# Optimization experiments

Hardware: AMD Instinct MI355X
Metric: run time of the kernel (lower is better)

The kernel has to match this reference:

```python
import jax, jax.numpy as jnp
import numpy as np

B, N, E = 512, 714, 4096
VOCAB = 400 + 38333   # cat_len + poi_len
ED = (128 - 3) // 2   # 62
F_IN = 2 * ED + 3     # 127


def setup_inputs() -> dict:
    key = jax.random.key(0)
    ks = jax.random.split(key, 16)
    s = 0.05
    return {
        "ids": jax.random.randint(ks[0], (B, N, 2), 0, VOCAB),
        "cont": jax.random.normal(ks[1], (B, N, 3), jnp.float32),
        "edges": jax.random.randint(ks[2], (B, 2, E), 0, N),
        "emb_table": jax.random.normal(ks[3], (VOCAB, ED), jnp.float32) * 0.02,
        "W1": jax.random.normal(ks[4], (F_IN, 32), jnp.float32) * s,
        "b1": jnp.zeros((32,), jnp.float32),
        "W2": jax.random.normal(ks[5], (32, 32), jnp.float32) * s,
        "b2": jnp.zeros((32,), jnp.float32),
        "W3": jax.random.normal(ks[6], (32, 32), jnp.float32) * s,
        "b3": jnp.zeros((32,), jnp.float32),
        "W4": jax.random.normal(ks[7], (32, 1), jnp.float32) * s,
        "b4": jnp.zeros((1,), jnp.float32),
        "Wf1": jax.random.normal(ks[8], (N, 128), jnp.float32) * s,
        "bf1": jnp.zeros((128,), jnp.float32),
        "Wf2": jax.random.normal(ks[9], (128, 128), jnp.float32) * s,
        "bf2": jnp.zeros((128,), jnp.float32),
    }


def _prep_edges(e):
    # PyG GCNConv: add self-loops, symmetric normalization
    loop = jnp.arange(N)
    row = jnp.concatenate([e[0], loop])           # source j
    col = jnp.concatenate([e[1], loop])           # target i
    deg = jnp.zeros((N,), jnp.float32).at[col].add(1.0)
    dinv = jax.lax.rsqrt(deg)                     # deg >= 1 (self-loops)
    return row, col, dinv[row] * dinv[col]


def _gcn(x, row, col, norm, W, b):
    # x: [N, F_in] -> [N, F_out]; gather-normalize-scatter aggregation
    xw = x @ W
    out = jnp.zeros_like(xw).at[col].add(xw[row] * norm[:, None])
    return out + b


_gcn_b = jax.vmap(_gcn, in_axes=(0, 0, 0, 0, None, None))


def _forward(ids, cont, edges, emb_table, W1, b1, W2, b2, W3, b3, W4, b4,
             Wf1, bf1, Wf2, bf2):
    lrelu = jax.nn.leaky_relu  # torch default slope 0.01
    emb = emb_table[ids.astype(jnp.int32)].reshape(B, N, 2 * ED)  # [B,N,124]
    x = jnp.concatenate([emb, cont], axis=-1)                      # [B,N,127]
    row, col, norm = jax.vmap(_prep_edges)(edges)
    h = lrelu(_gcn_b(x, row, col, norm, W1, b1))
    t = _gcn_b(h, row, col, norm, W2, b2)
    h = lrelu(t) + t
    t = _gcn_b(h, row, col, norm, W3, b3)
    h = lrelu(t) + t
    h = lrelu(_gcn_b(h, row, col, norm, W4, b4))                   # [B,N,1]
    h = h.reshape(B, N)
    h = jax.nn.relu(h @ Wf1 + bf1)
    return jax.nn.relu(h @ Wf2 + bf2)                              # [B,128]


def reference(ids, cont, edges, emb_table, W1, b1, W2, b2, W3, b3, W4, b4,
              Wf1, bf1, Wf2, bf2):
    return _forward(ids, cont, edges, emb_table, W1, b1, W2, b2, W3, b3,
                    W4, b4, Wf1, bf1, Wf2, bf2)
```

## Files before the change

### kernel.cpp

```cpp
#include <hip/hip_runtime.h>
#include <hip/hip_bf16.h>

#define BB 512
#define NN 714
#define EE 4096
#define ED2 62
#define CH 32
#define NT16 45
#define NPAD 720
#define VOCAB 38733
#define NPRE 303
#define ELLR 432
#define ELLB (ELLR*16)

typedef unsigned int u32;
typedef unsigned short u16;
typedef short short8 __attribute__((ext_vector_type(8)));
typedef float float4v __attribute__((ext_vector_type(4)));
typedef _Float16 f16x2 __attribute__((ext_vector_type(2)));
typedef __fp16 fp16x2 __attribute__((ext_vector_type(2)));

__device__ __forceinline__ u32 f2bf(float f) {
  u32 u = __float_as_uint(f);
  return (u + 0x7fffu + ((u >> 16) & 1u)) >> 16;
}
__device__ __forceinline__ u32 pack2(float a, float b) {
  return f2bf(a) | (f2bf(b) << 16);
}
__device__ __forceinline__ f16x2 u2h(u32 x) { union { u32 u; f16x2 h; } c; c.u = x; return c.h; }
__device__ __forceinline__ u32 packh(float a, float b) {
  union { fp16x2 h; u32 u; } c;
  c.h = __builtin_amdgcn_cvt_pkrtz(a, b);
  return c.u;
}

__device__ __forceinline__ int yslot(int node, int q) {
  return (node << 2) | (q ^ ((node >> 1) & 3));
}

__global__ __launch_bounds__(256) void k_setup(const float* __restrict__ emb,
    const float* __restrict__ W1, u32* __restrict__ Tg,
    const int* __restrict__ edges,
    float* __restrict__ dinv, u16* __restrict__ perm_g,
    u16* __restrict__ ell_g, u16* __restrict__ elloff_g)
{
  const int tid = threadIdx.x;
  if (blockIdx.x < NPRE) {
    const int base = blockIdx.x * 128;
    const int lane = tid & 63, wv = tid >> 6;
    const int col = lane & 15, kg = lane >> 4;
    __shared__ __align__(16) unsigned short sX[128 * 64];
    for (int s = tid; s < 1024; s += 256) {
      const int row = s >> 3, ck = s & 7;
      uint4 w = {0, 0, 0, 0};
      if (base + row < VOCAB) {
        const float2* __restrict__ p = (const float2*)(emb + (size_t)(base + row) * ED2 + ck * 8);
        float2 v0 = p[0], v1 = p[1], v2 = p[2];
        float2 v3; v3.x = 0.f; v3.y = 0.f;
        if (ck != 7) v3 = p[3];
        w.x = pack2(v0.x, v0.y); w.y = pack2(v1.x, v1.y);
        w.z = pack2(v2.x, v2.y); w.w = pack2(v3.x, v3.y);
      }
      ((uint4*)sX)[(row * 8 + ck) ^ (row & 7)] = w;
    }
    union { u32 u[4]; short8 v; } A[2][4];
#pragma unroll
    for (int kc = 0; kc < 2; ++kc)
#pragma unroll
      for (int hh = 0; hh < 4; ++hh) {
        const int tbl = hh >> 1;
        const int ch = ((hh & 1) * 16) + col;
#pragma unroll
        for (int jj = 0; jj < 4; ++jj) {
          const int k0 = kc * 32 + kg * 8 + 2 * jj;
          const int k1 = k0 + 1;
          const float wa = (k0 < 62) ? W1[(tbl * 62 + k0) * CH + ch] : 0.f;
          const float wb = (k1 < 62) ? W1[(tbl * 62 + k1) * CH + ch] : 0.f;
          A[kc][hh].u[jj] = pack2(wa, wb);
        }
      }
    __syncthreads();
    for (int t = wv; t < 8; t += 4) {
      const int ln = t * 16 + col;
      float4v acc[4];
#pragma unroll
      for (int hh = 0; hh < 4; ++hh) { acc[hh][0] = 0.f; acc[hh][1] = 0.f; acc[hh][2] = 0.f; acc[hh][3] = 0.f; }
#pragma unroll
      for (int kc = 0; kc < 2; ++kc) {
        const int idx8 = (ln * 8 + kc * 4 + kg) ^ (ln & 7);
        short8 bf = *(const short8*)(sX + idx8 * 8);
#pragma unroll
        for (int hh = 0; hh < 4; ++hh)
          acc[hh] = __builtin_amdgcn_mfma_f32_16x16x32_bf16(A[kc][hh].v, bf, acc[hh], 0, 0, 0);
      }
      const int row = base + ln;
      if (row < VOCAB) {
        u32* op = Tg + (size_t)row * 32;
#pragma unroll
        for (int hh = 0; hh < 4; ++hh) {
          uint2 s0 = { packh(acc[hh][0], acc[hh][1]), packh(acc[hh][2], acc[hh][3]) };
          *(uint2*)(op + hh * 8 + 2 * kg) = s0;
        }
      }
    }
    return;
  }
  const int b = blockIdx.x - NPRE;
  const int* __restrict__ er = edges + (size_t)b * 2 * EE;
  const int* __restrict__ ec = er + EE;
  __shared__ int s_cnt[NN];
  __shared__ int s_a[1024];
  __shared__ int s_b[1024];
  __shared__ u16 s_rows16[EE];
  __shared__ u16 s_perm[NPAD];
  __shared__ u16 s_degP[NPAD];
  __shared__ int s_hist[64];
  __shared__ int s_md[NT16 + 1];

  for (int i = tid; i < NN; i += 256) s_cnt[i] = 0;
  __syncthreads();
  for (int e = tid; e < EE; e += 256) atomicAdd(&s_cnt[ec[e]], 1);
  __syncthreads();
  for (int i = tid; i < 1024; i += 256) s_a[i] = (i < NN) ? s_cnt[i] : 0;
  for (int i = tid; i < NN; i += 256)
    dinv[(size_t)b * NN + i] = rsqrtf((float)(s_cnt[i] + 1));
  __syncthreads();
  int* src = s_a; int* dst = s_b;
  for (int d = 1; d < 1024; d <<= 1) {
    for (int i = tid; i < 1024; i += 256) {
      int v = src[i];
      if (i >= d) v += src[i - d];
      dst[i] = v;
    }
    __syncthreads();
    int* t = src; src = dst; dst = t;
  }
  for (int i = tid; i < NN; i += 256) s_cnt[i] = 0;
  __syncthreads();
  for (int e = tid; e < EE; e += 256) {
    int c = ec[e];
    int p = atomicAdd(&s_cnt[c], 1);
    int base = (c == 0) ? 0 : src[c - 1];
    s_rows16[base + p] = (u16)er[e];
  }
  for (int i = tid; i < 64; i += 256) s_hist[i] = 0;
  for (int i = tid; i < NPAD; i += 256) { s_perm[i] = 0xFFFFu; s_degP[i] = 0; }
  __syncthreads();
  for (int i = tid; i < NN; i += 256) {
    int deg = src[i] - (i ? src[i - 1] : 0);
    atomicAdd(&s_hist[deg < 63 ? deg : 63], 1);
  }
  __syncthreads();
  if (tid < 64) {
    int v = s_hist[tid];
    int incl = v;
#pragma unroll
    for (int d = 1; d < 64; d <<= 1) {
      int o = __shfl_up(incl, d, 64);
      if (tid >= d) incl += o;
    }
    s_hist[tid] = incl - v;
  }
  __syncthreads();
  for (int i = tid; i < NN; i += 256) {
    int deg = src[i] - (i ? src[i - 1] : 0);
    int pos = atomicAdd(&s_hist[deg < 63 ? deg : 63], 1);
    s_perm[pos] = (u16)i;
    s_degP[pos] = (u16)deg;
  }
  __syncthreads();
  for (int i = tid; i < NPAD; i += 256) perm_g[(size_t)b * NPAD + i] = s_perm[i];
  if (tid < NT16) {
    int md = 0;
#pragma unroll
    for (int c = 0; c < 16; ++c) { int d = s_degP[tid * 16 + c]; md = d > md ? d : md; }
    s_md[tid] = (md + 3) & ~3;
  }
  __syncthreads();
  if (tid < 64) {
    int m = (tid < NT16) ? s_md[tid] : 0;
    int incl = m;
#pragma unroll
    for (int d = 1; d < 64; d <<= 1) {
      int o = __shfl_up(incl, d, 64);
      if (tid >= d) incl += o;
    }
    int excl = incl - m;
    if (excl > ELLR) excl = ELLR;
    if (tid < NT16) s_md[tid] = excl;
    if (tid == NT16 - 1) s_md[NT16] = (incl > ELLR) ? ELLR : incl;
  }
  __syncthreads();
  if (tid <= NT16) elloff_g[(size_t)b * (NT16 + 1) + tid] = (u16)s_md[tid];
  {
    const int wv4 = tid >> 6, lane = tid & 63;
    u16* eg = ell_g + (size_t)b * ELLB;
    for (int t = wv4; t < NT16; t += 4) {
      const int base = s_md[t], md4 = s_md[t + 1] - base;
      for (int s = lane; s < md4 * 16; s += 64) {
        const int kk = s >> 4, col = s & 15;
        const int pv = s_perm[t * 16 + col];
        int r = NN;
        if (pv != 0xFFFF) {
          const int deg = s_degP[t * 16 + col];
          if (kk < deg) {
            const int off = pv ? src[pv - 1] : 0;
            r = (int)s_rows16[off + kk];
          }
        }
        eg[base * 16 + s] = (u16)((r << 2) | ((r >> 1) & 3));
      }
    }
  }
}

#define EDGEA(EP, K) { const int a16 = ((int)(EP)[(K) * 16]) ^ kg; \
  uint4 n = sy4[a16]; \
  a0h += u2h(n.x); a1h += u2h(n.y); a2h += u2h(n.z); a3h += u2h(n.w); }
#define EDGEB(EP, K) { const int a16 = ((int)(EP)[(K) * 16]) ^ kg; \
  uint4 n = sy4[a16]; \
  b0h += u2h(n.x); b1h += u2h(n.y); b2h += u2h(n.z); b3h += u2h(n.w); }
#define FLUSH { a0h += b0h; a1h += b1h; a2h += b2h; a3h += b3h; \
  zx[0] += (float)a0h.x; zx[1] += (float)a0h.y; \
  zx[2] += (float)a1h.x; zx[3] += (float)a1h.y; \
  zx[4] += (float)a2h.x; zx[5] += (float)a2h.y; \
  zx[6] += (float)a3h.x; zx[7] += (float)a3h.y; \
  a0h = hz; a1h = hz; a2h = hz; a3h = hz; \
  b0h = hz; b1h = hz; b2h = hz; b3h = hz; }
#define AGG_LOOP(EP) { int kk = 0; \
  while (kk + 16 <= md4) { \
    _Pragma("unroll") for (int e = 0; e < 16; e += 2) { EDGEA(EP, kk + e) EDGEB(EP, kk + e + 1) } \
    FLUSH \
    kk += 16; } \
  if (kk + 8 <= md4) { \
    _Pragma("unroll") for (int e = 0; e < 8; e += 2) { EDGEA(EP, kk + e) EDGEB(EP, kk + e + 1) } \
    FLUSH \
    kk += 8; } \
  if (kk < md4) { \
    _Pragma("unroll") for (int e = 0; e < 4; e += 2) { EDGEA(EP, kk + e) EDGEB(EP, kk + e + 1) } \
    FLUSH } }

template<int ACT>
__device__ __forceinline__ void gcn_pass32(
    u32* __restrict__ sy, const u16* __restrict__ s_ell,
    const u16* __restrict__ s_elloff, const float* __restrict__ s_dv,
    const u16* __restrict__ pvs,
    const int wv, const int col, const int kg,
    const short8 a0v, const short8 a1v, const float* __restrict__ bias8)
{
  const uint4* sy4 = (const uint4*)sy;
  const f16x2 hz = {(_Float16)0, (_Float16)0};
  u32 outs[3][4];
  int nodes[3];
#pragma unroll
  for (int p = 0; p < 3; ++p) {
    const int t = p * 16 + wv;
    const int pv = (t < NT16) ? (int)pvs[p] : 0xFFFF;
    const int node = (pv == 0xFFFF) ? NN : pv;
    nodes[p] = (pv == 0xFFFF) ? -1 : pv;
    int base = 0, md4 = 0;
    if (t < NT16) { base = s_elloff[t]; md4 = s_elloff[t + 1] - base; }
    base = __builtin_amdgcn_readfirstlane(base);
    md4 = __builtin_amdgcn_readfirstlane(md4);
    f16x2 a0h, a1h, a2h, a3h;
    f16x2 b0h = hz, b1h = hz, b2h = hz, b3h = hz;
    {
      uint4 u = sy4[yslot(node, kg)];
      a0h = u2h(u.x); a1h = u2h(u.y); a2h = u2h(u.z); a3h = u2h(u.w);
    }
    float zx[8];
#pragma unroll
    for (int j = 0; j < 8; ++j) zx[j] = 0.f;
    const u16* ep = s_ell + base * 16 + col;
    AGG_LOOP(ep)
    const float dv = s_dv[node];
    float h[8];
#pragma unroll
    for (int j = 0; j < 8; ++j) {
      float t2 = fmaf(dv, zx[j], bias8[j]);
      float l = (t2 > 0.f) ? t2 : 0.01f * t2;
      h[j] = (ACT == 0) ? l : (l + t2);
    }
    union { u32 u[4]; short8 v; } ub;
#pragma unroll
    for (int jj = 0; jj < 4; ++jj) ub.u[jj] = pack2(h[2 * jj], h[2 * jj + 1]);
    float4v z4 = {0.f, 0.f, 0.f, 0.f};
    float4v d0 = __builtin_amdgcn_mfma_f32_16x16x32_bf16(a0v, ub.v, z4, 0, 0, 0);
    float4v d1 = __builtin_amdgcn_mfma_f32_16x16x32_bf16(a1v, ub.v, z4, 0, 0, 0);
    outs[p][0] = packh(d0[0] * dv, d0[1] * dv);
    outs[p][1] = packh(d0[2] * dv, d0[3] * dv);
    outs[p][2] = packh(d1[0] * dv, d1[1] * dv);
    outs[p][3] = packh(d1[2] * dv, d1[3] * dv);
  }
  __syncthreads();
#pragma unroll
  for (int p = 0; p < 3; ++p) {
    const int node = nodes[p];
    if (node >= 0) {
      const int sw = (node >> 1) & 3;
      u32* op = sy + node * 16;
      uint2 s0 = { outs[p][0], outs[p][1] };
      uint2 s1 = { outs[p][2], outs[p][3] };
      *(uint2*)(op + (((kg >> 1) ^ sw) << 2) + ((2 * kg) & 3)) = s0;
      *(uint2*)(op + (((2 + (kg >> 1)) ^ sw) << 2) + ((2 * kg) & 3)) = s1;
    }
  }
  __syncthreads();
}

__global__ __launch_bounds__(1024) void k_fused(
    const int* __restrict__ ids, const float* __restrict__ cont,
    const u32* __restrict__ T, const float* __restrict__ W1,
    const float* __restrict__ dinv,
    const u16* __restrict__ perm_g, const u16* __restrict__ ell_g,
    const u16* __restrict__ elloff_g,
    const float* __restrict__ b1, const float* __restrict__ W2,
    const float* __restrict__ b2, const float* __restrict__ W3,
    const float* __restrict__ b3, const float* __restrict__ W4,
    const float* __restrict__ b4, const float* __restrict__ Wf1,
    const float* __restrict__ bf1, const float* __restrict__ Wf2,
    const float* __restrict__ bf2, float* __restrict__ out)
{
  const int b = blockIdx.x;
  const int tid = threadIdx.x;
  const int lane = tid & 63;
  const int wv = tid >> 6;
  const int col = lane & 15;
  const int kg = lane >> 4;

  __shared__ __align__(16) char smem[65408];
  u32*   s_y      = (u32*)smem;
  u16*   s_ell    = (u16*)(smem + 45760);
  u16*   s_elloff = (u16*)(smem + 59584);
  float* s_dv     = (float*)(smem + 59680);
  float* s_h      = (float*)(smem + 62544);
  float* s_red    = (float*)smem;
  float* s_u      = (float*)(smem + 8192);

  {
    const uint4 z4 = {0, 0, 0, 0};
    uint4* sy4w = (uint4*)s_y;
    if (tid < 4) sy4w[yslot(NN, tid)] = z4;
    const uint4* __restrict__ esrc = (const uint4*)(ell_g + (size_t)b * ELLB);
    uint4* ed = (uint4*)s_ell;
    for (int s = tid; s < ELLB / 8; s += 1024) ed[s] = esrc[s];
    for (int i = tid; i <= NT16; i += 1024) s_elloff[i] = elloff_g[(size_t)b * (NT16 + 1) + i];
    for (int i = tid; i < NN; i += 1024) s_dv[i] = dinv[(size_t)b * NN + i];
    if (tid == 1023) s_dv[NN] = 0.f;
    if (tid < 96) s_h[tid] = W1[124 * 32 + tid];
  }
  __syncthreads();
  if (tid < NN) {
    const int node = tid;
    const int2 id2 = ((const int2*)ids)[(size_t)b * NN + node];
    const uint4* __restrict__ t0 = (const uint4*)(T + (size_t)id2.x * 32);
    const uint4* __restrict__ t1 = (const uint4*)(T + (size_t)id2.y * 32 + 16);
    uint4 q0 = t0[0], q1 = t0[1], q2 = t0[2], q3 = t0[3];
    uint4 r0 = t1[0], r1 = t1[1], r2 = t1[2], r3 = t1[3];
    const float* __restrict__ c3 = cont + ((size_t)b * NN + node) * 3;
    const float c0 = c3[0], c1 = c3[1], c2 = c3[2];
    const float dv = s_dv[node];
    const u32 qs[16] = { q0.x, q0.y, q0.z, q0.w, q1.x, q1.y, q1.z, q1.w,
                         q2.x, q2.y, q2.z, q2.w, q3.x, q3.y, q3.z, q3.w };
    const u32 rs[16] = { r0.x, r0.y, r0.z, r0.w, r1.x, r1.y, r1.z, r1.w,
                         r2.x, r2.y, r2.z, r2.w, r3.x, r3.y, r3.z, r3.w };
    u32 os[16];
#pragma unroll
    for (int s = 0; s < 16; ++s) {
      f16x2 a = u2h(qs[s]);
      f16x2 bb = u2h(rs[s]);
      const int ch = 2 * s;
      float v0 = (float)a.x + (float)bb.x;
      float v1 = (float)a.y + (float)bb.y;
      v0 = fmaf(c0, s_h[ch],      v0);
      v1 = fmaf(c0, s_h[ch + 1],  v1);
      v0 = fmaf(c1, s_h[32 + ch],     v0);
      v1 = fmaf(c1, s_h[32 + ch + 1], v1);
      v0 = fmaf(c2, s_h[64 + ch],     v0);
      v1 = fmaf(c2, s_h[64 + ch + 1], v1);
      os[s] = packh(v0 * dv, v1 * dv);
    }
    uint4* sy4w = (uint4*)s_y;
#pragma unroll
    for (int s4 = 0; s4 < 4; ++s4) {
      uint4 w = { os[4 * s4], os[4 * s4 + 1], os[4 * s4 + 2], os[4 * s4 + 3] };
      sy4w[yslot(node, s4)] = w;
    }
  }
  u16 pvs[3];
#pragma unroll
  for (int p = 0; p < 3; ++p) {
    const int t = p * 16 + wv;
    pvs[p] = (t < NT16) ? perm_g[(size_t)b * NPAD + t * 16 + col] : (u16)0xFFFF;
  }
  const u16 pvt = (tid < NPAD) ? perm_g[(size_t)b * NPAD + tid] : (u16)0xFFFF;

  union { u32 u[4]; short8 v; } uaA0, uaA1, uaB0, uaB1;
#pragma unroll
  for (int jj = 0; jj < 4; ++jj) {
    uaA0.u[jj] = pack2(W2[(kg * 8 + 2 * jj) * CH + col],      W2[(kg * 8 + 2 * jj + 1) * CH + col]);
    uaA1.u[jj] = pack2(W2[(kg * 8 + 2 * jj) * CH + 16 + col], W2[(kg * 8 + 2 * jj + 1) * CH + 16 + col]);
    uaB0.u[jj] = pack2(W3[(kg * 8 + 2 * jj) * CH + col],      W3[(kg * 8 + 2 * jj + 1) * CH + col]);
    uaB1.u[jj] = pack2(W3[(kg * 8 + 2 * jj) * CH + 16 + col], W3[(kg * 8 + 2 * jj + 1) * CH + 16 + col]);
  }
  float b1r[8], b2r[8], b3r[8], w4r[8];
#pragma unroll
  for (int j = 0; j < 8; ++j) {
    b1r[j] = b1[kg * 8 + j];
    b2r[j] = b2[kg * 8 + j];
    b3r[j] = b3[kg * 8 + j];
    w4r[j] = W4[kg * 8 + j];
  }
  const float bb4 = b4[0];
  __syncthreads();

  gcn_pass32<0>(s_y, s_ell, s_elloff, s_dv, pvs, wv, col, kg, uaA0.v, uaA1.v, b1r);
  gcn_pass32<1>(s_y, s_ell, s_elloff, s_dv, pvs, wv, col, kg, uaB0.v, uaB1.v, b2r);

  {
    const uint4* sy4 = (const uint4*)s_y;
    const f16x2 hz = {(_Float16)0, (_Float16)0};
#pragma unroll
    for (int p = 0; p < 3; ++p) {
      const int t = p * 16 + wv;
      const int pv = (t < NT16) ? (int)pvs[p] : 0xFFFF;
      const int node = (pv == 0xFFFF) ? NN : pv;
      int base = 0, md4 = 0;
      if (t < NT16) { base = s_elloff[t]; md4 = s_elloff[t + 1] - base; }
      base = __builtin_amdgcn_readfirstlane(base);
      md4 = __builtin_amdgcn_readfirstlane(md4);
      f16x2 a0h, a1h, a2h, a3h;
      f16x2 b0h = hz, b1h = hz, b2h = hz, b3h = hz;
      {
        uint4 u = sy4[yslot(node, kg)];
        a0h = u2h(u.x); a1h = u2h(u.y); a2h = u2h(u.z); a3h = u2h(u.w);
      }
      float zx[8];
#pragma unroll
      for (int j = 0; j < 8; ++j) zx[j] = 0.f;
      const u16* ep = s_ell + base * 16 + col;
      AGG_LOOP(ep)
      const float dv = s_dv[node];
      float part = 0.f;
#pragma unroll
      for (int j = 0; j < 8; ++j) {
        float t2 = fmaf(dv, zx[j], b3r[j]);
        float l = (t2 > 0.f) ? t2 : 0.01f * t2;
        part = fmaf(l + t2, w4r[j], part);
      }
      part += __shfl_xor(part, 16, 64);
      part += __shfl_xor(part, 32, 64);
      if (pv != 0xFFFF && kg == 0) s_h[node] = part * dv;
    }
  }
  __syncthreads();
  if (tid == 1023) s_h[NN] = 0.f;
  __syncthreads();

  {
    float hval = 0.f;
    int node = -1;
    if (tid < NPAD && pvt != 0xFFFF) {
      node = (int)pvt;
      const int t = tid >> 4, c = tid & 15;
      const int base = s_elloff[t], md4 = s_elloff[t + 1] - base;
      float z = s_h[node];
      const u16* ep = s_ell + base * 16 + c;
      for (int kk = 0; kk < md4; ++kk) z += s_h[((int)ep[kk * 16]) >> 2];
      float t2 = fmaf(s_dv[node], z, bb4);
      hval = (t2 > 0.f) ? t2 : 0.01f * t2;
    }
    __syncthreads();
    if (node >= 0) s_h[node] = hval;
  }
  __syncthreads();

  const int j = tid & 127, q = tid >> 7;
  {
    const int n0 = (q * NN) >> 3, n1 = ((q + 1) * NN) >> 3;
    const float* __restrict__ w = Wf1 + j;
    float a0 = 0.f, a1 = 0.f;
    int n = n0;
#pragma unroll 4
    for (; n + 2 <= n1; n += 2) {
      a0 = fmaf(s_h[n], w[(size_t)n * 128], a0);
      a1 = fmaf(s_h[n + 1], w[(size_t)(n + 1) * 128], a1);
    }
    if (n < n1) a0 = fmaf(s_h[n], w[(size_t)n * 128], a0);
    s_red[tid] = a0 + a1;
  }
  __syncthreads();
  if (tid < 128) {
    float v = bf1[tid];
#pragma unroll
    for (int m = 0; m < 8; ++m) v += s_red[tid + 128 * m];
    s_u[tid] = fmaxf(v, 0.f);
  }
  __syncthreads();
  {
    const float* __restrict__ w = Wf2 + j;
    float a0 = 0.f, a1 = 0.f;
#pragma unroll
    for (int k = q * 16; k < q * 16 + 16; k += 2) {
      a0 = fmaf(s_u[k], w[(size_t)k * 128], a0);
      a1 = fmaf(s_u[k + 1], w[(size_t)(k + 1) * 128], a1);
    }
    s_red[tid] = a0 + a1;
  }
  __syncthreads();
  if (tid < 128) {
    float v = bf2[tid];
#pragma unroll
    for (int m = 0; m < 8; ++m) v += s_red[tid + 128 * m];
    out[(size_t)b * 128 + tid] = fmaxf(v, 0.f);
  }
}

extern "C" void kernel_launch(void* const* d_in, const int* in_sizes, int n_in,
                              void* d_out, int out_size, void* d_ws, size_t ws_size,
                              hipStream_t stream)
{
  (void)in_sizes; (void)n_in; (void)out_size; (void)ws_size;
  const int*   ids  = (const int*)d_in[0];
  const float* cont = (const float*)d_in[1];
  const int*   edges= (const int*)d_in[2];
  const float* emb  = (const float*)d_in[3];
  const float* W1   = (const float*)d_in[4];
  const float* b1   = (const float*)d_in[5];
  const float* W2   = (const float*)d_in[6];
  const float* b2   = (const float*)d_in[7];
  const float* W3   = (const float*)d_in[8];
  const float* b3   = (const float*)d_in[9];
  const float* W4   = (const float*)d_in[10];
  const float* b4   = (const float*)d_in[11];
  const float* Wf1  = (const float*)d_in[12];
  const float* bf1  = (const float*)d_in[13];
  const float* Wf2  = (const float*)d_in[14];
  const float* bf2  = (const float*)d_in[15];
  float* out = (float*)d_out;

  char* ws = (char*)d_ws;
  size_t off = 0;
  auto alloc = [&](size_t bytes) -> void* {
    void* p = ws + off;
    off = (off + bytes + 255) & ~(size_t)255;
    return p;
  };
  float* dinv     = (float*)alloc((size_t)BB * NN * 4);
  u16*   perm     = (u16*)  alloc((size_t)BB * NPAD * 2);
  u16*   ell      = (u16*)  alloc((size_t)BB * ELLB * 2);
  u16*   elloff   = (u16*)  alloc((size_t)BB * (NT16 + 1) * 2);
  u32*   T        = (u32*)  alloc((size_t)VOCAB * 32 * 4);

  hipLaunchKernelGGL(k_setup, dim3(NPRE + BB), dim3(256), 0, stream,
                     emb, W1, T, edges, dinv, perm, ell, elloff);
  hipLaunchKernelGGL(k_fused, dim3(BB), dim3(1024), 0, stream,
                     ids, cont, T, W1, dinv, perm, ell, elloff,
                     b1, W2, b2, W3, b3, W4, b4, Wf1, bf1, Wf2, bf2, out);
}
```

Baseline: 88.38 us.

## Fuse per-graph edge preprocessing into main kernel, building ELL in shared memory

The per-graph degree count, CSR build, degree-sorted permutation and ELL construction move from the setup kernel into the fused per-graph kernel, reusing shared memory before the node-feature phase. This removes global writes and reads of dinv, perm, ELL and offsets, and shrinks the setup launch to only the embedding-table projection. The prefix scan is now done with wave shuffles over 1024 threads. In exchange the fused kernel's serial prologue grows, shared memory moves to a slightly larger dynamic allocation, and the edge work no longer overlaps the table-projection blocks.

After: 83.18 us. 1.06x faster.

```diff
diff --git a/kernel.cpp b/kernel.cpp
--- a/kernel.cpp
+++ b/kernel.cpp
@@ -12,6 +12,7 @@
 #define NPRE 303
 #define ELLR 432
 #define ELLB (ELLR*16)
+#define DYN_LDS 66848
 
 typedef unsigned int u32;
 typedef unsigned short u16;
@@ -39,176 +40,63 @@
 }
 
 __global__ __launch_bounds__(256) void k_setup(const float* __restrict__ emb,
-    const float* __restrict__ W1, u32* __restrict__ Tg,
-    const int* __restrict__ edges,
-    float* __restrict__ dinv, u16* __restrict__ perm_g,
-    u16* __restrict__ ell_g, u16* __restrict__ elloff_g)
+    const float* __restrict__ W1, u32* __restrict__ Tg)
 {
   const int tid = threadIdx.x;
-  if (blockIdx.x < NPRE) {
-    const int base = blockIdx.x * 128;
-    const int lane = tid & 63, wv = tid >> 6;
-    const int col = lane & 15, kg = lane >> 4;
-    __shared__ __align__(16) unsigned short sX[128 * 64];
-    for (int s = tid; s < 1024; s += 256) {
-      const int row = s >> 3, ck = s & 7;
-      uint4 w = {0, 0, 0, 0};
-      if (base + row < VOCAB) {
-        const float2* __restrict__ p = (const float2*)(emb + (size_t)(base + row) * ED2 + ck * 8);
-        float2 v0 = p[0], v1 = p[1], v2 = p[2];
-        float2 v3; v3.x = 0.f; v3.y = 0.f;
-        if (ck != 7) v3 = p[3];
-        w.x = pack2(v0.x, v0.y); w.y = pack2(v1.x, v1.y);
-        w.z = pack2(v2.x, v2.y); w.w = pack2(v3.x, v3.y);
-      }
-      ((uint4*)sX)[(row * 8 + ck) ^ (row & 7)] = w;
-    }
-    union { u32 u[4]; short8 v; } A[2][4];
-#pragma unroll
-    for (int kc = 0; kc < 2; ++kc)
+  const int base = blockIdx.x * 128;
+  const int lane = tid & 63, wv = tid >> 6;
+  const int col = lane & 15, kg = lane >> 4;
+  __shared__ __align__(16) unsigned short sX[128 * 64];
+  for (int s = tid; s < 1024; s += 256) {
+    const int row = s >> 3, ck = s & 7;
+    uint4 w = {0, 0, 0, 0};
+    if (base + row < VOCAB) {
+      const float2* __restrict__ p = (const float2*)(emb + (size_t)(base + row) * ED2 + ck * 8);
+      float2 v0 = p[0], v1 = p[1], v2 = p[2];
+      float2 v3; v3.x = 0.f; v3.y = 0.f;
+      if (ck != 7) v3 = p[3];
+      w.x = pack2(v0.x, v0.y); w.y = pack2(v1.x, v1.y);
+      w.z = pack2(v2.x, v2.y); w.w = pack2(v3.x, v3.y);
+    }
+    ((uint4*)sX)[(row * 8 + ck) ^ (row & 7)] = w;
+  }
+  union { u32 u[4]; short8 v; } A[2][4];
+#pragma unroll
+  for (int kc = 0; kc < 2; ++kc)
+#pragma unroll
+    for (int hh = 0; hh < 4; ++hh) {
+      const int tbl = hh >> 1;
+      const int ch = ((hh & 1) * 16) + col;
+#pragma unroll
+      for (int jj = 0; jj < 4; ++jj) {
+        const int k0 = kc * 32 + kg * 8 + 2 * jj;
+        const int k1 = k0 + 1;
+        const float wa = (k0 < 62) ? W1[(tbl * 62 + k0) * CH + ch] : 0.f;
+        const float wb = (k1 < 62) ? W1[(tbl * 62 + k1) * CH + ch] : 0.f;
+        A[kc][hh].u[jj] = pack2(wa, wb);
+      }
+    }
+  __syncthreads();
+  for (int t = wv; t < 8; t += 4) {
+    const int ln = t * 16 + col;
+    float4v acc[4];
+#pragma unroll
+    for (int hh = 0; hh < 4; ++hh) { acc[hh][0] = 0.f; acc[hh][1] = 0.f; acc[hh][2] = 0.f; acc[hh][3] = 0.f; }
+#pragma unroll
+    for (int kc = 0; kc < 2; ++kc) {
+      const int idx8 = (ln * 8 + kc * 4 + kg) ^ (ln & 7);
+      short8 bf = *(const short8*)(sX + idx8 * 8);
+#pragma unroll
+      for (int hh = 0; hh < 4; ++hh)
+        acc[hh] = __builtin_amdgcn_mfma_f32_16x16x32_bf16(A[kc][hh].v, bf, acc[hh], 0, 0, 0);
+    }
+    const int row = base + ln;
+    if (row < VOCAB) {
+      u32* op = Tg + (size_t)row * 32;
 #pragma unroll
       for (int hh = 0; hh < 4; ++hh) {
-        const int tbl = hh >> 1;
-        const int ch = ((hh & 1) * 16) + col;
-#pragma unroll
-        for (int jj = 0; jj < 4; ++jj) {
-          const int k0 = kc * 32 + kg * 8 + 2 * jj;
-          const int k1 = k0 + 1;
-          const float wa = (k0 < 62) ? W1[(tbl * 62 + k0) * CH + ch] : 0.f;
-          const float wb = (k1 < 62) ? W1[(tbl * 62 + k1) * CH + ch] : 0.f;
-          A[kc][hh].u[jj] = pack2(wa, wb);
-        }
-      }
-    __syncthreads();
-    for (int t = wv; t < 8; t += 4) {
-      const int ln = t * 16 + col;
-      float4v acc[4];
-#pragma unroll
-      for (int hh = 0; hh < 4; ++hh) { acc[hh][0] = 0.f; acc[hh][1] = 0.f; acc[hh][2] = 0.f; acc[hh][3] = 0.f; }
-#pragma unroll
-      for (int kc = 0; kc < 2; ++kc) {
-        const int idx8 = (ln * 8 + kc * 4 + kg) ^ (ln & 7);
-        short8 bf = *(const short8*)(sX + idx8 * 8);
-#pragma unroll
-        for (int hh = 0; hh < 4; ++hh)
-          acc[hh] = __builtin_amdgcn_mfma_f32_16x16x32_bf16(A[kc][hh].v, bf, acc[hh], 0, 0, 0);
-      }
-      const int row = base + ln;
-      if (row < VOCAB) {
-        u32* op = Tg + (size_t)row * 32;
-#pragma unroll
-        for (int hh = 0; hh < 4; ++hh) {
-          uint2 s0 = { packh(acc[hh][0], acc[hh][1]), packh(acc[hh][2], acc[hh][3]) };
-          *(uint2*)(op + hh * 8 + 2 * kg) = s0;
-        }
-      }
-    }
-    return;
-  }
-  const int b = blockIdx.x - NPRE;
-  const int* __restrict__ er = edges + (size_t)b * 2 * EE;
-  const int* __restrict__ ec = er + EE;
-  __shared__ int s_cnt[NN];
-  __shared__ int s_a[1024];
-  __shared__ int s_b[1024];
-  __shared__ u16 s_rows16[EE];
-  __shared__ u16 s_perm[NPAD];
-  __shared__ u16 s_degP[NPAD];
-  __shared__ int s_hist[64];
-  __shared__ int s_md[NT16 + 1];
-
-  for (int i = tid; i < NN; i += 256) s_cnt[i] = 0;
-  __syncthreads();
-  for (int e = tid; e < EE; e += 256) atomicAdd(&s_cnt[ec[e]], 1);
-  __syncthreads();
-  for (int i = tid; i < 1024; i += 256) s_a[i] = (i < NN) ? s_cnt[i] : 0;
-  for (int i = tid; i < NN; i += 256)
-    dinv[(size_t)b * NN + i] = rsqrtf((float)(s_cnt[i] + 1));
-  __syncthreads();
-  int* src = s_a; int* dst = s_b;
-  for (int d = 1; d < 1024; d <<= 1) {
-    for (int i = tid; i < 1024; i += 256) {
-      int v = src[i];
-      if (i >= d) v += src[i - d];
-      dst[i] = v;
-    }
-    __syncthreads();
-    int* t = src; src = dst; dst = t;
-  }
-  for (int i = tid; i < NN; i += 256) s_cnt[i] = 0;
-  __syncthreads();
-  for (int e = tid; e < EE; e += 256) {
-    int c = ec[e];
-    int p = atomicAdd(&s_cnt[c], 1);
-    int base = (c == 0) ? 0 : src[c - 1];
-    s_rows16[base + p] = (u16)er[e];
-  }
-  for (int i = tid; i < 64; i += 256) s_hist[i] = 0;
-  for (int i = tid; i < NPAD; i += 256) { s_perm[i] = 0xFFFFu; s_degP[i] = 0; }
-  __syncthreads();
-  for (int i = tid; i < NN; i += 256) {
-    int deg = src[i] - (i ? src[i - 1] : 0);
-    atomicAdd(&s_hist[deg < 63 ? deg : 63], 1);
-  }
-  __syncthreads();
-  if (tid < 64) {
-    int v = s_hist[tid];
-    int incl = v;
-#pragma unroll
-    for (int d = 1; d < 64; d <<= 1) {
-      int o = __shfl_up(incl, d, 64);
-      if (tid >= d) incl += o;
-    }
-    s_hist[tid] = incl - v;
-  }
-  __syncthreads();
-  for (int i = tid; i < NN; i += 256) {
-    int deg = src[i] - (i ? src[i - 1] : 0);
-    int pos = atomicAdd(&s_hist[deg < 63 ? deg : 63], 1);
-    s_perm[pos] = (u16)i;
-    s_degP[pos] = (u16)deg;
-  }
-  __syncthreads();
-  for (int i = tid; i < NPAD; i += 256) perm_g[(size_t)b * NPAD + i] = s_perm[i];
-  if (tid < NT16) {
-    int md = 0;
-#pragma unroll
-    for (int c = 0; c < 16; ++c) { int d = s_degP[tid * 16 + c]; md = d > md ? d : md; }
-    s_md[tid] = (md + 3) & ~3;
-  }
-  __syncthreads();
-  if (tid < 64) {
-    int m = (tid < NT16) ? s_md[tid] : 0;
-    int incl = m;
-#pragma unroll
-    for (int d = 1; d < 64; d <<= 1) {
-      int o = __shfl_up(incl, d, 64);
-      if (tid >= d) incl += o;
-    }
-    int excl = incl - m;
-    if (excl > ELLR) excl = ELLR;
-    if (tid < NT16) s_md[tid] = excl;
-    if (tid == NT16 - 1) s_md[NT16] = (incl > ELLR) ? ELLR : incl;
-  }
-  __syncthreads();
-  if (tid <= NT16) elloff_g[(size_t)b * (NT16 + 1) + tid] = (u16)s_md[tid];
-  {
-    const int wv4 = tid >> 6, lane = tid & 63;
-    u16* eg = ell_g + (size_t)b * ELLB;
-    for (int t = wv4; t < NT16; t += 4) {
-      const int base = s_md[t], md4 = s_md[t + 1] - base;
-      for (int s = lane; s < md4 * 16; s += 64) {
-        const int kk = s >> 4, col = s & 15;
-        const int pv = s_perm[t * 16 + col];
-        int r = NN;
-        if (pv != 0xFFFF) {
-          const int deg = s_degP[t * 16 + col];
-          if (kk < deg) {
-            const int off = pv ? src[pv - 1] : 0;
-            r = (int)s_rows16[off + kk];
-          }
-        }
-        eg[base * 16 + s] = (u16)((r << 2) | ((r >> 1) & 3));
+        uint2 s0 = { packh(acc[hh][0], acc[hh][1]), packh(acc[hh][2], acc[hh][3]) };
+        *(uint2*)(op + hh * 8 + 2 * kg) = s0;
       }
     }
   }
@@ -310,10 +198,8 @@
 
 __global__ __launch_bounds__(1024) void k_fused(
     const int* __restrict__ ids, const float* __restrict__ cont,
+    const int* __restrict__ edges,
     const u32* __restrict__ T, const float* __restrict__ W1,
-    const float* __restrict__ dinv,
-    const u16* __restrict__ perm_g, const u16* __restrict__ ell_g,
-    const u16* __restrict__ elloff_g,
     const float* __restrict__ b1, const float* __restrict__ W2,
     const float* __restrict__ b2, const float* __restrict__ W3,
     const float* __restrict__ b3, const float* __restrict__ W4,
@@ -328,72 +214,173 @@
   const int col = lane & 15;
   const int kg = lane >> 4;
 
-  __shared__ __align__(16) char smem[65408];
+  extern __shared__ __align__(16) char smem[];
   u32*   s_y      = (u32*)smem;
   u16*   s_ell    = (u16*)(smem + 45760);
   u16*   s_elloff = (u16*)(smem + 59584);
   float* s_dv     = (float*)(smem + 59680);
   float* s_h      = (float*)(smem + 62544);
+  u16*   s_perm   = (u16*)(smem + 65408);
   float* s_red    = (float*)smem;
   float* s_u      = (float*)(smem + 8192);
-
+  int*   s_cnt    = (int*)smem;
+  int*   s_csr    = (int*)(smem + 2944);
+  u16*   s_rows16 = (u16*)(smem + 5888);
+  u16*   s_degP   = (u16*)(smem + 14080);
+  int*   s_md     = (int*)(smem + 15520);
+  int*   s_wsum   = (int*)(smem + 15776);
+
+  const int* __restrict__ er = edges + (size_t)b * 2 * EE;
+  const int* __restrict__ ec = er + EE;
+  for (int i = tid; i < NN; i += 1024) s_cnt[i] = 0;
+  if (tid < 96) s_h[tid] = W1[124 * 32 + tid];
+  __syncthreads();
+  for (int e = tid; e < EE; e += 1024) atomicAdd(&s_cnt[ec[e]], 1);
+  __syncthreads();
+  const int deg = (tid < NN) ? s_cnt[tid] : 0;
+  if (tid < NN) s_dv[tid] = rsqrtf((float)(deg + 1));
+  if (tid == 0) s_dv[NN] = 0.f;
   {
-    const uint4 z4 = {0, 0, 0, 0};
+    int incl = deg;
+#pragma unroll
+    for (int d = 1; d < 64; d <<= 1) {
+      int o = __shfl_up(incl, d, 64);
+      if (lane >= d) incl += o;
+    }
+    if (lane == 63) s_wsum[wv] = incl;
+    __syncthreads();
+    if (wv == 0 && lane < 16) {
+      int v = s_wsum[lane];
+      int ic = v;
+#pragma unroll
+      for (int d = 1; d < 16; d <<= 1) {
+        int o = __shfl_up(ic, d, 16);
+        if (lane >= d) ic += o;
+      }
+      s_wsum[lane] = ic - v;
+    }
+    __syncthreads();
+    incl += s_wsum[wv];
+    if (tid < NN) s_csr[tid] = incl;
+  }
+  __syncthreads();
+  for (int i = tid; i < NN; i += 1024) s_cnt[i] = 0;
+  __syncthreads();
+  for (int e = tid; e < EE; e += 1024) {
+    const int c = ec[e];
+    const int p = atomicAdd(&s_cnt[c], 1);
+    const int off = c ? s_csr[c - 1] : 0;
+    s_rows16[off + p] = (u16)er[e];
+  }
+  if (tid < 64) s_md[tid] = 0;
+  for (int i = tid; i < NPAD; i += 1024) { s_perm[i] = 0xFFFFu; s_degP[i] = 0; }
+  __syncthreads();
+  if (tid < NN) atomicAdd(&s_md[deg < 63 ? deg : 63], 1);
+  __syncthreads();
+  if (tid < 64) {
+    int v = s_md[tid];
+    int incl = v;
+#pragma unroll
+    for (int d = 1; d < 64; d <<= 1) {
+      int o = __shfl_up(incl, d, 64);
+      if (tid >= d) incl += o;
+    }
+    s_md[tid] = incl - v;
+  }
+  __syncthreads();
+  if (tid < NN) {
+    const int pos = atomicAdd(&s_md[deg < 63 ? deg : 63], 1);
+    s_perm[pos] = (u16)tid;
+    s_degP[pos] = (u16)deg;
+  }
+  __syncthreads();
+  if (tid < NT16) {
+    int md = 0;
+#pragma unroll
+    for (int c = 0; c < 16; ++c) { int d = s_degP[tid * 16 + c]; md = d > md ? d : md; }
+    s_md[tid] = (md + 3) & ~3;
+  }
+  __syncthreads();
+  if (tid < 64) {
+    int m = (tid < NT16) ? s_md[tid] : 0;
+    int incl = m;
+#pragma unroll
+    for (int d = 1; d < 64; d <<= 1) {
+      int o = __shfl_up(incl, d, 64);
+      if (tid >= d) incl += o;
+    }
+    int excl = incl - m;
+    if (excl > ELLR) excl = ELLR;
+    if (tid < NT16) s_md[tid] = excl;
+    if (tid == NT16 - 1) s_md[NT16] = (incl > ELLR) ? ELLR : incl;
+  }
+  __syncthreads();
+  if (tid <= NT16) s_elloff[tid] = (u16)s_md[tid];
+  for (int t = wv; t < NT16; t += 16) {
+    const int base = s_md[t], md4 = s_md[t + 1] - base;
+    for (int s = lane; s < md4 * 16; s += 64) {
+      const int kk = s >> 4, c = s & 15;
+      const int pv = s_perm[t * 16 + c];
+      int r = NN;
+      if (pv != 0xFFFF) {
+        const int dg = s_degP[t * 16 + c];
+        if (kk < dg) {
+          const int off = pv ? s_csr[pv - 1] : 0;
+          r = (int)s_rows16[off + kk];
+        }
+      }
+      s_ell[base * 16 + s] = (u16)((r << 2) | ((r >> 1) & 3));
+    }
+  }
+  __syncthreads();
+
+  {
     uint4* sy4w = (uint4*)s_y;
-    if (tid < 4) sy4w[yslot(NN, tid)] = z4;
-    const uint4* __restrict__ esrc = (const uint4*)(ell_g + (size_t)b * ELLB);
-    uint4* ed = (uint4*)s_ell;
-    for (int s = tid; s < ELLB / 8; s += 1024) ed[s] = esrc[s];
-    for (int i = tid; i <= NT16; i += 1024) s_elloff[i] = elloff_g[(size_t)b * (NT16 + 1) + i];
-    for (int i = tid; i < NN; i += 1024) s_dv[i] = dinv[(size_t)b * NN + i];
-    if (tid == 1023) s_dv[NN] = 0.f;
-    if (tid < 96) s_h[tid] = W1[124 * 32 + tid];
-  }
-  __syncthreads();
-  if (tid < NN) {
-    const int node = tid;
-    const int2 id2 = ((const int2*)ids)[(size_t)b * NN + node];
-    const uint4* __restrict__ t0 = (const uint4*)(T + (size_t)id2.x * 32);
-    const uint4* __restrict__ t1 = (const uint4*)(T + (size_t)id2.y * 32 + 16);
-    uint4 q0 = t0[0], q1 = t0[1], q2 = t0[2], q3 = t0[3];
-    uint4 r0 = t1[0], r1 = t1[1], r2 = t1[2], r3 = t1[3];
-    const float* __restrict__ c3 = cont + ((size_t)b * NN + node) * 3;
-    const float c0 = c3[0], c1 = c3[1], c2 = c3[2];
-    const float dv = s_dv[node];
-    const u32 qs[16] = { q0.x, q0.y, q0.z, q0.w, q1.x, q1.y, q1.z, q1.w,
-                         q2.x, q2.y, q2.z, q2.w, q3.x, q3.y, q3.z, q3.w };
-    const u32 rs[16] = { r0.x, r0.y, r0.z, r0.w, r1.x, r1.y, r1.z, r1.w,
-                         r2.x, r2.y, r2.z, r2.w, r3.x, r3.y, r3.z, r3.w };
-    u32 os[16];
-#pragma unroll
-    for (int s = 0; s < 16; ++s) {
-      f16x2 a = u2h(qs[s]);
-      f16x2 bb = u2h(rs[s]);
-      const int ch = 2 * s;
-      float v0 = (float)a.x + (float)bb.x;
-      float v1 = (float)a.y + (float)bb.y;
-      v0 = fmaf(c0, s_h[ch],      v0);
-      v1 = fmaf(c0, s_h[ch + 1],  v1);
-      v0 = fmaf(c1, s_h[32 + ch],     v0);
-      v1 = fmaf(c1, s_h[32 + ch + 1], v1);
-      v0 = fmaf(c2, s_h[64 + ch],     v0);
-      v1 = fmaf(c2, s_h[64 + ch + 1], v1);
-      os[s] = packh(v0 * dv, v1 * dv);
-    }
-    uint4* sy4w = (uint4*)s_y;
-#pragma unroll
-    for (int s4 = 0; s4 < 4; ++s4) {
-      uint4 w = { os[4 * s4], os[4 * s4 + 1], os[4 * s4 + 2], os[4 * s4 + 3] };
-      sy4w[yslot(node, s4)] = w;
+    if (tid < 4) { const uint4 z4 = {0, 0, 0, 0}; sy4w[yslot(NN, tid)] = z4; }
+    if (tid < NN) {
+      const int node = tid;
+      const int2 id2 = ((const int2*)ids)[(size_t)b * NN + node];
+      const uint4* __restrict__ t0 = (const uint4*)(T + (size_t)id2.x * 32);
+      const uint4* __restrict__ t1 = (const uint4*)(T + (size_t)id2.y * 32 + 16);
+      uint4 q0 = t0[0], q1 = t0[1], q2 = t0[2], q3 = t0[3];
+      uint4 r0 = t1[0], r1 = t1[1], r2 = t1[2], r3 = t1[3];
+      const float* __restrict__ c3 = cont + ((size_t)b * NN + node) * 3;
+      const float c0 = c3[0], c1 = c3[1], c2 = c3[2];
+      const float dv = s_dv[node];
+      const u32 qs[16] = { q0.x, q0.y, q0.z, q0.w, q1.x, q1.y, q1.z, q1.w,
+                           q2.x, q2.y, q2.z, q2.w, q3.x, q3.y, q3.z, q3.w };
+      const u32 rs[16] = { r0.x, r0.y, r0.z, r0.w, r1.x, r1.y, r1.z, r1.w,
+                           r2.x, r2.y, r2.z, r2.w, r3.x, r3.y, r3.z, r3.w };
+      u32 os[16];
+#pragma unroll
+      for (int s = 0; s < 16; ++s) {
+        f16x2 a = u2h(qs[s]);
+        f16x2 bb = u2h(rs[s]);
+        const int ch = 2 * s;
+        float v0 = (float)a.x + (float)bb.x;
+        float v1 = (float)a.y + (float)bb.y;
+        v0 = fmaf(c0, s_h[ch],      v0);
+        v1 = fmaf(c0, s_h[ch + 1],  v1);
+        v0 = fmaf(c1, s_h[32 + ch],     v0);
+        v1 = fmaf(c1, s_h[32 + ch + 1], v1);
+        v0 = fmaf(c2, s_h[64 + ch],     v0);
+        v1 = fmaf(c2, s_h[64 + ch + 1], v1);
+        os[s] = packh(v0 * dv, v1 * dv);
+      }
+#pragma unroll
+      for (int s4 = 0; s4 < 4; ++s4) {
+        uint4 w = { os[4 * s4], os[4 * s4 + 1], os[4 * s4 + 2], os[4 * s4 + 3] };
+        sy4w[yslot(node, s4)] = w;
+      }
     }
   }
   u16 pvs[3];
 #pragma unroll
   for (int p = 0; p < 3; ++p) {
     const int t = p * 16 + wv;
-    pvs[p] = (t < NT16) ? perm_g[(size_t)b * NPAD + t * 16 + col] : (u16)0xFFFF;
-  }
-  const u16 pvt = (tid < NPAD) ? perm_g[(size_t)b * NPAD + tid] : (u16)0xFFFF;
+    pvs[p] = (t < NT16) ? s_perm[t * 16 + col] : (u16)0xFFFF;
+  }
+  const u16 pvt = (tid < NPAD) ? s_perm[tid] : (u16)0xFFFF;
 
   union { u32 u[4]; short8 v; } uaA0, uaA1, uaB0, uaB1;
 #pragma unroll
@@ -546,15 +533,10 @@
     off = (off + bytes + 255) & ~(size_t)255;
     return p;
   };
-  float* dinv     = (float*)alloc((size_t)BB * NN * 4);
-  u16*   perm     = (u16*)  alloc((size_t)BB * NPAD * 2);
-  u16*   ell      = (u16*)  alloc((size_t)BB * ELLB * 2);
-  u16*   elloff   = (u16*)  alloc((size_t)BB * (NT16 + 1) * 2);
-  u32*   T        = (u32*)  alloc((size_t)VOCAB * 32 * 4);
-
-  hipLaunchKernelGGL(k_setup, dim3(NPRE + BB), dim3(256), 0, stream,
-                     emb, W1, T, edges, dinv, perm, ell, elloff);
-  hipLaunchKernelGGL(k_fused, dim3(BB), dim3(1024), 0, stream,
-                     ids, cont, T, W1, dinv, perm, ell, elloff,
+  u32* T = (u32*)alloc((size_t)VOCAB * 32 * 4);
+
+  hipLaunchKernelGGL(k_setup, dim3(NPRE), dim3(256), 0, stream, emb, W1, T);
+  hipLaunchKernelGGL(k_fused, dim3(BB), dim3(1024), DYN_LDS, stream,
+                     ids, cont, edges, T, W1,
                      b1, W2, b2, W3, b3, W4, b4, Wf1, bf1, Wf2, bf2, out);
 }
```
